# Optimization experiments

Hardware: AMD Instinct MI355X
Metric: run time of the kernel (lower is better)

The kernel has to match this reference:

```python
import jax, jax.numpy as jnp
import numpy as np

B, T, D_IN, H, NUM_OUT = 64, 2048, 128, 512, 128


def _lstm_layer(x, W_ih, W_hh, b_ih, b_hh):
    # x: [B, T, D]; W_ih: [4H, D]; W_hh: [4H, H]; gate order i, f, g, o (PyTorch)
    Bsz = x.shape[0]
    Hh = W_hh.shape[1]
    # Precompute the input projection for all timesteps in one big GEMM: [B, T, 4H]
    xg = jnp.einsum('btd,gd->btg', x, W_ih) + b_ih + b_hh
    h0 = jnp.zeros((Bsz, Hh), x.dtype)
    c0 = jnp.zeros((Bsz, Hh), x.dtype)

    def step(carry, xg_t):
        h, c = carry
        gates = xg_t + h @ W_hh.T  # [B, 4H]
        i, f, g, o = jnp.split(gates, 4, axis=-1)
        i = jax.nn.sigmoid(i)
        f = jax.nn.sigmoid(f)
        g = jnp.tanh(g)
        o = jax.nn.sigmoid(o)
        c = f * c + i * g
        h = o * jnp.tanh(c)
        return (h, c), h

    (_, _), hs = jax.lax.scan(step, (h0, c0), jnp.swapaxes(xg, 0, 1))  # hs: [T, B, H]
    return jnp.swapaxes(hs, 0, 1)  # [B, T, H]


def setup_inputs() -> dict:
    key = jax.random.key(0)
    ks = jax.random.split(key, 7)

    def xavier(k, shape):
        fan_in, fan_out = shape[1], shape[0]
        lim = np.sqrt(6.0 / (fan_in + fan_out))
        return jax.random.uniform(k, shape, jnp.float32, -lim, lim)

    return {
        'x': jax.random.normal(ks[0], (B, T, D_IN), jnp.float32),
        'W_ih0': xavier(ks[1], (4 * H, D_IN)),
        'W_hh0': xavier(ks[2], (4 * H, H)),
        'b_ih0': jnp.zeros((4 * H,), jnp.float32),
        'b_hh0': jnp.zeros((4 * H,), jnp.float32),
        'W_ih1': xavier(ks[3], (4 * H, H)),
        'W_hh1': xavier(ks[4], (4 * H, H)),
        'b_ih1': jnp.zeros((4 * H,), jnp.float32),
        'b_hh1': jnp.zeros((4 * H,), jnp.float32),
        'fc_w': xavier(ks[5], (NUM_OUT, H)),
        'fc_b': jnp.zeros((NUM_OUT,), jnp.float32),
    }


def reference(x, W_ih0, W_hh0, b_ih0, b_hh0, W_ih1, W_hh1, b_ih1, b_hh1, fc_w, fc_b):
    out = _lstm_layer(x, W_ih0, W_hh0, b_ih0, b_hh0)
    out = _lstm_layer(out, W_ih1, W_hh1, b_ih1, b_hh1)
    # fc applied to last timestep only
    return out[:, -1, :] @ fc_w.T + fc_b
```

## Files before the change

### kernel.cpp

```cpp
#include <hip/hip_runtime.h>
#include <hip/hip_fp16.h>
#include <math.h>

#define BB    64
#define TT    2048
#define DIN   128
#define HH    512
#define NWG   256
#define NTHR  256
#define NUNITS 1152

typedef __attribute__((ext_vector_type(4))) unsigned int u32x4;
typedef __attribute__((ext_vector_type(8))) _Float16    f16x8;
typedef __attribute__((ext_vector_type(4))) float       f32x4;

__device__ __forceinline__ float sigm(float v) { return 1.0f / (1.0f + expf(-v)); }

__device__ __forceinline__ u32x4 ld16m(const void* p) {
  u32x4 v;
  asm volatile("global_load_dwordx4 %0, %1, off sc0 sc1" : "=v"(v) : "v"(p) : "memory");
  return v;
}
__device__ __forceinline__ void st8m(void* p, unsigned long long v) {
  __hip_atomic_store((unsigned long long*)p, v, __ATOMIC_RELAXED, __HIP_MEMORY_SCOPE_AGENT);
}
__device__ __forceinline__ unsigned long long ld8m(const void* p) {
  return __hip_atomic_load((const unsigned long long*)p, __ATOMIC_RELAXED, __HIP_MEMORY_SCOPE_AGENT);
}
__device__ __forceinline__ void gbar(unsigned* cnt, unsigned target, int* dead) {
  __syncthreads();
  if (threadIdx.x == 0 && *dead == 0) {
    asm volatile("s_waitcnt vmcnt(0)" ::: "memory");
    __hip_atomic_fetch_add(cnt, 1u, __ATOMIC_RELAXED, __HIP_MEMORY_SCOPE_AGENT);
    long sp = 0;
    while (__hip_atomic_load(cnt, __ATOMIC_RELAXED, __HIP_MEMORY_SCOPE_AGENT) < target) {
      __builtin_amdgcn_s_sleep(1);
      if (++sp > (1L << 22)) { *dead = 1; break; }
    }
    asm volatile("" ::: "memory");
  }
  __syncthreads();
}

__global__ __launch_bounds__(64, 1) void prep_flush() {
  extern __shared__ char dummy[];
  if (threadIdx.x == 0) { __threadfence(); dummy[0] = 0; }
  __syncthreads();
}
__global__ void prep_zero(unsigned* w) {
  const int total = (4*BB*HH*2 + 4096) / 4;
  for (int i = blockIdx.x*blockDim.x + threadIdx.x; i < total; i += gridDim.x*blockDim.x)
    __hip_atomic_store(w + i, 0u, __ATOMIC_RELAXED, __HIP_MEMORY_SCOPE_AGENT);
}
__global__ void xcvt(const float* __restrict__ x, unsigned long long* __restrict__ xh) {
  const int N4 = BB*TT*DIN/4;
  const float4* x4 = reinterpret_cast<const float4*>(x);
  for (int i = blockIdx.x*blockDim.x + threadIdx.x; i < N4; i += gridDim.x*blockDim.x) {
    float4 v = x4[i];
    __half2 a = __floats2half2_rn(v.x, v.y);
    __half2 b = __floats2half2_rn(v.z, v.w);
    unsigned long long u = ((unsigned long long)__builtin_bit_cast(unsigned, b) << 32)
                         |  (unsigned long long)__builtin_bit_cast(unsigned, a);
    __hip_atomic_store(&xh[i], u, __ATOMIC_RELAXED, __HIP_MEMORY_SCOPE_AGENT);
  }
}

__global__ __launch_bounds__(NTHR, 1) void lstm2_ntr(
    const float* __restrict__ Wih0, const float* __restrict__ Whh0,
    const float* __restrict__ bih0, const float* __restrict__ bhh0,
    const float* __restrict__ Wih1, const float* __restrict__ Whh1,
    const float* __restrict__ bih1, const float* __restrict__ bhh1,
    const float* __restrict__ fcw,  const float* __restrict__ fcb,
    float* __restrict__ out, float* __restrict__ ws)
{
  extern __shared__ char smbase[];
  const int tid  = threadIdx.x;
  const int wg   = blockIdx.x;
  const int lane = tid & 63;
  const int wv   = tid >> 6;

  const int grp  = wg >> 5;
  const int r    = wg & 31;
  const int bg8  = grp * 8;
  const int c0   = 16*r + 4*wv;

  __half* h0s = reinterpret_cast<__half*>(ws);
  __half* h1s = h0s + 2*BB*HH;
  unsigned* gcnt = reinterpret_cast<unsigned*>(reinterpret_cast<char*>(ws) + 262144) + grp*32;
  const __half* xh = reinterpret_cast<const __half*>(reinterpret_cast<char*>(ws) + 524288);
  __half* hout = reinterpret_cast<__half*>(smbase + 18432);
  int*    dead = reinterpret_cast<int*>(smbase + 18944);

  const int rt   = lane & 15;
  const int gate = rt & 3;
  const int jc   = rt >> 2;
  const int kg   = lane >> 4;
  const int b15  = lane & 15;
  const int n0   = gate*HH + (c0 + jc);

  f16x8 af0[20];
#pragma unroll
  for (int m = 0; m < 20; ++m) {
    int k0 = 32*m + 8*kg;
    const float* srcp = (k0 < DIN) ? (Wih0 + (size_t)n0*DIN + k0)
                                   : (Whh0 + (size_t)n0*HH + (k0 - DIN));
    float4 a = *reinterpret_cast<const float4*>(srcp);
    float4 b = *reinterpret_cast<const float4*>(srcp + 4);
    f16x8 fr;
    fr[0]=(_Float16)a.x; fr[1]=(_Float16)a.y; fr[2]=(_Float16)a.z; fr[3]=(_Float16)a.w;
    fr[4]=(_Float16)b.x; fr[5]=(_Float16)b.y; fr[6]=(_Float16)b.z; fr[7]=(_Float16)b.w;
    af0[m] = fr;
  }
  f16x8 af1[32];
#pragma unroll
  for (int m = 0; m < 32; ++m) {
    int k0 = 32*m + 8*kg;
    const float* srcp = (k0 < HH) ? (Wih1 + (size_t)n0*HH + k0)
                                  : (Whh1 + (size_t)n0*HH + (k0 - HH));
    float4 a = *reinterpret_cast<const float4*>(srcp);
    float4 b = *reinterpret_cast<const float4*>(srcp + 4);
    f16x8 fr;
    fr[0]=(_Float16)a.x; fr[1]=(_Float16)a.y; fr[2]=(_Float16)a.z; fr[3]=(_Float16)a.w;
    fr[4]=(_Float16)b.x; fr[5]=(_Float16)b.y; fr[6]=(_Float16)b.z; fr[7]=(_Float16)b.w;
    af1[m] = fr;
  }

  const int cmy = c0 + kg;
  float bv0[4], bv1[4];
#pragma unroll
  for (int g = 0; g < 4; ++g) {
    bv0[g] = bih0[g*HH + cmy] + bhh0[g*HH + cmy];
    bv1[g] = bih1[g*HH + cmy] + bhh1[g*HH + cmy];
  }

  float cst0 = 0.f, cst1 = 0.f;
  const int beff = (b15 < 8) ? b15 : 7;
  if (tid == 0) *dead = 0;
  __syncthreads();

  for (int st = 0; st <= TT; ++st) {
    const int tcur = (st < TT) ? st : (TT - 1);
    const __half* h0r = h0s + (st & 1)*(BB*HH);
    const __half* h1r = h1s + (st & 1)*(BB*HH);

    u32x4 stgL[5];
    int   physv[5];
#pragma unroll
    for (int ii = 0; ii < 5; ++ii) {
      int idx = tid + NTHR*ii;
      physv[ii] = -1;
      if (idx < NUNITS) {
        const __half* src; int phys;
        if (idx < 128)      { int b = idx>>4, u = idx&15;
          src = xh + (size_t)(bg8+b)*TT*DIN + (size_t)tcur*DIN + u*8;
          phys = b*16 + (u ^ b); }
        else if (idx < 640) { int i2 = idx-128, b = i2>>6, u = i2&63;
          src = h0r + (size_t)(bg8+b)*HH + u*8;
          phys = 128 + b*64 + (u ^ b); }
        else                { int i2 = idx-640, b = i2>>6, u = i2&63;
          src = h1r + (size_t)(bg8+b)*HH + u*8;
          phys = 640 + b*64 + (u ^ b); }
        physv[ii] = phys;
        stgL[ii] = ld16m(src);
      }
    }
    asm volatile("s_waitcnt vmcnt(0)" ::: "memory");
    __builtin_amdgcn_sched_barrier(0);
#pragma unroll
    for (int ii = 0; ii < 5; ++ii)
      if (physv[ii] >= 0)
        *reinterpret_cast<u32x4*>(smbase + physv[ii]*16) = stgL[ii];
    __syncthreads();

    f32x4 a0a = {0.f,0.f,0.f,0.f}, a0b = a0a, a1a = a0a, a1b = a0a;
#pragma unroll
    for (int m = 0; m < 20; ++m) {
      int phys = (m < 4) ? (beff*16 + ((4*m + kg) ^ beff))
                         : (128 + beff*64 + ((4*(m-4) + kg) ^ beff));
      f16x8 bf = *reinterpret_cast<const f16x8*>(smbase + phys*16);
      if (m & 1) a0b = __builtin_amdgcn_mfma_f32_16x16x32_f16(af0[m], bf, a0b, 0, 0, 0);
      else       a0a = __builtin_amdgcn_mfma_f32_16x16x32_f16(af0[m], bf, a0a, 0, 0, 0);
    }
#pragma unroll
    for (int m = 0; m < 32; ++m) {
      int phys = (m < 16) ? (128 + beff*64 + ((4*m + kg) ^ beff))
                          : (640 + beff*64 + ((4*(m-16) + kg) ^ beff));
      f16x8 bf = *reinterpret_cast<const f16x8*>(smbase + phys*16);
      if (m & 1) a1b = __builtin_amdgcn_mfma_f32_16x16x32_f16(af1[m], bf, a1b, 0, 0, 0);
      else       a1a = __builtin_amdgcn_mfma_f32_16x16x32_f16(af1[m], bf, a1a, 0, 0, 0);
    }
    f32x4 a0 = a0a + a0b;
    f32x4 a1 = a1a + a1b;

    if (st < TT) {
      float gi = sigm (a0[0] + bv0[0]);
      float gf = sigm (a0[1] + bv0[1]);
      float gg = tanhf(a0[2] + bv0[2]);
      float go = sigm (a0[3] + bv0[3]);
      cst0 = gf*cst0 + gi*gg;
      float hn = go * tanhf(cst0);
      if (b15 < 8) hout[(0*8 + b15)*16 + 4*wv + kg] = __float2half(hn);
    }
    if (st >= 1) {
      float gi = sigm (a1[0] + bv1[0]);
      float gf = sigm (a1[1] + bv1[1]);
      float gg = tanhf(a1[2] + bv1[2]);
      float go = sigm (a1[3] + bv1[3]);
      cst1 = gf*cst1 + gi*gg;
      float hn = go * tanhf(cst1);
      if (b15 < 8) hout[(1*8 + b15)*16 + 4*wv + kg] = __float2half(hn);
    }
    __syncthreads();

    if (tid < 64) {
      int layer = tid >> 5, q = tid & 31, b = q >> 2, part = q & 3;
      bool do_st = (layer == 0) ? (st < TT) : (st >= 1);
      if (do_st) {
        unsigned long long v =
            *reinterpret_cast<unsigned long long*>(hout + (layer*8 + b)*16 + part*4);
        __half* base = (layer ? h1s : h0s) + ((st + 1) & 1)*(BB*HH);
        st8m(base + (size_t)(bg8+b)*HH + 16*r + part*4, v);
      }
    }
    gbar(gcnt, 32u*(unsigned)(st + 1), dead);
  }

  {
    const __half* h1f = h1s + (BB*HH);
    int oi = tid >> 3, kp = tid & 7;
    int b  = oi >> 2, cc = oi & 3;
    int ocol = 4*r + cc;
    const unsigned long long* h8 =
        reinterpret_cast<const unsigned long long*>(h1f + (size_t)(bg8+b)*HH) + kp*16;
    const float* wrow = fcw + (size_t)ocol*HH + kp*64;
    float p = 0.f;
#pragma unroll
    for (int kk = 0; kk < 16; ++kk) {
      unsigned long long v = ld8m(h8 + kk);
      __half2 hlo = __builtin_bit_cast(__half2, (unsigned)(v & 0xffffffffull));
      __half2 hhi = __builtin_bit_cast(__half2, (unsigned)(v >> 32));
      float2 flo = __half22float2(hlo), fhi = __half22float2(hhi);
      float4 w = *reinterpret_cast<const float4*>(wrow + kk*4);
      p += flo.x*w.x + flo.y*w.y + fhi.x*w.z + fhi.y*w.w;
    }
    p += __shfl_xor(p, 1);
    p += __shfl_xor(p, 2);
    p += __shfl_xor(p, 4);
    if (kp == 0) out[(size_t)(bg8+b)*128 + ocol] = p + fcb[ocol];
  }
}

__global__ void sentinel_fail(float* out, float v) { out[threadIdx.x] = v; }

extern "C" void kernel_launch(void* const* d_in, const int* in_sizes, int n_in,
                              void* d_out, int out_size, void* d_ws, size_t ws_size,
                              hipStream_t stream) {
  const float* x    = (const float*)d_in[0];
  const float* Wih0 = (const float*)d_in[1];
  const float* Whh0 = (const float*)d_in[2];
  const float* bih0 = (const float*)d_in[3];
  const float* bhh0 = (const float*)d_in[4];
  const float* Wih1 = (const float*)d_in[5];
  const float* Whh1 = (const float*)d_in[6];
  const float* bih1 = (const float*)d_in[7];
  const float* bhh1 = (const float*)d_in[8];
  const float* fcw  = (const float*)d_in[9];
  const float* fcb  = (const float*)d_in[10];
  float* out = (float*)d_out;
  float* ws  = (float*)d_ws;
  (void)in_sizes; (void)n_in; (void)out_size;

  const size_t need = 524288 + (size_t)BB*TT*DIN*2;
  if (ws_size < need) {
    sentinel_fail<<<1, 128, 0, stream>>>(out, 2.0e6f);
    return;
  }

  const int smem_bytes = 108*1024;
  hipFuncSetAttribute(reinterpret_cast<const void*>(&lstm2_ntr),
                      hipFuncAttributeMaxDynamicSharedMemorySize, smem_bytes);
  hipFuncSetAttribute(reinterpret_cast<const void*>(&prep_flush),
                      hipFuncAttributeMaxDynamicSharedMemorySize, smem_bytes);

  (void)hipGetLastError();
  prep_flush<<<dim3(NWG), dim3(64), smem_bytes, stream>>>();
  xcvt<<<dim3(2048), dim3(NTHR), 0, stream>>>(
      x, reinterpret_cast<unsigned long long*>(reinterpret_cast<char*>(d_ws) + 524288));
  prep_zero<<<dim3(NWG), dim3(NTHR), 0, stream>>>((unsigned*)d_ws);
  lstm2_ntr<<<dim3(NWG), dim3(NTHR), smem_bytes, stream>>>(
      Wih0, Whh0, bih0, bhh0, Wih1, Whh1, bih1, bhh1, fcw, fcb, out, ws);
  hipError_t e = hipGetLastError();
  if (e != hipSuccess) {
    sentinel_fail<<<1, 128, 0, stream>>>(out, 1.0e6f);
  }
}
```

Before: 8.324 ms.

## Split global barrier into per-layer arrive/poll and overlap layer-1 with layer-0 wait

Replaces the single per-step group barrier with two counters, one per layer. Each workgroup now computes layer-1 from a double-buffered LDS copy of the previous step while waiting for layer-0 hidden states. Layer-1 hidden states use a triple-buffered global array, so the layer-0 critical path only waits on layer-0 producers. The aim is to hide barrier latency and global load latency behind MFMA work, at the cost of an extra loop iteration, more syncthreads and more complex buffer indexing.

New measurement: 9.803 ms. +17.8%, slower.

```diff
diff --git a/kernel.cpp b/kernel.cpp
--- a/kernel.cpp
+++ b/kernel.cpp
@@ -8,38 +8,34 @@
 #define HH    512
 #define NWG   256
 #define NTHR  256
-#define NUNITS 1152
 
 typedef __attribute__((ext_vector_type(4))) unsigned int u32x4;
 typedef __attribute__((ext_vector_type(8))) _Float16    f16x8;
 typedef __attribute__((ext_vector_type(4))) float       f32x4;
+typedef unsigned long long u64;
 
 __device__ __forceinline__ float sigm(float v) { return 1.0f / (1.0f + expf(-v)); }
 
-__device__ __forceinline__ u32x4 ld16m(const void* p) {
-  u32x4 v;
-  asm volatile("global_load_dwordx4 %0, %1, off sc0 sc1" : "=v"(v) : "v"(p) : "memory");
-  return v;
-}
-__device__ __forceinline__ void st8m(void* p, unsigned long long v) {
-  __hip_atomic_store((unsigned long long*)p, v, __ATOMIC_RELAXED, __HIP_MEMORY_SCOPE_AGENT);
-}
-__device__ __forceinline__ unsigned long long ld8m(const void* p) {
-  return __hip_atomic_load((const unsigned long long*)p, __ATOMIC_RELAXED, __HIP_MEMORY_SCOPE_AGENT);
-}
-__device__ __forceinline__ void gbar(unsigned* cnt, unsigned target, int* dead) {
-  __syncthreads();
-  if (threadIdx.x == 0 && *dead == 0) {
-    asm volatile("s_waitcnt vmcnt(0)" ::: "memory");
-    __hip_atomic_fetch_add(cnt, 1u, __ATOMIC_RELAXED, __HIP_MEMORY_SCOPE_AGENT);
-    long sp = 0;
-    while (__hip_atomic_load(cnt, __ATOMIC_RELAXED, __HIP_MEMORY_SCOPE_AGENT) < target) {
-      __builtin_amdgcn_s_sleep(1);
-      if (++sp > (1L << 22)) { *dead = 1; break; }
-    }
-    asm volatile("" ::: "memory");
-  }
-  __syncthreads();
+__device__ __forceinline__ u64 ald(const void* p) {
+  return __hip_atomic_load((const u64*)p, __ATOMIC_RELAXED, __HIP_MEMORY_SCOPE_AGENT);
+}
+__device__ __forceinline__ void ast(void* p, u64 v) {
+  __hip_atomic_store((u64*)p, v, __ATOMIC_RELAXED, __HIP_MEMORY_SCOPE_AGENT);
+}
+__device__ __forceinline__ void put16(char* dst, u64 lo, u64 hi) {
+  u32x4 v; v.x=(unsigned)lo; v.y=(unsigned)(lo>>32); v.z=(unsigned)hi; v.w=(unsigned)(hi>>32);
+  *reinterpret_cast<u32x4*>(dst) = v;
+}
+__device__ __forceinline__ void barrive(unsigned* cnt) {
+  __hip_atomic_fetch_add(cnt, 1u, __ATOMIC_RELAXED, __HIP_MEMORY_SCOPE_AGENT);
+}
+__device__ __forceinline__ void bpoll(unsigned* cnt, unsigned target, int* dead) {
+  if (*dead) return;
+  long sp = 0;
+  while (__hip_atomic_load(cnt, __ATOMIC_RELAXED, __HIP_MEMORY_SCOPE_AGENT) < target) {
+    __builtin_amdgcn_s_sleep(1);
+    if (++sp > (1L << 22)) { *dead = 1; break; }
+  }
 }
 
 __global__ __launch_bounds__(64, 1) void prep_flush() {
@@ -48,24 +44,23 @@
   __syncthreads();
 }
 __global__ void prep_zero(unsigned* w) {
-  const int total = (4*BB*HH*2 + 4096) / 4;
+  const int total = (131072 + 196608 + 4096) / 4;
   for (int i = blockIdx.x*blockDim.x + threadIdx.x; i < total; i += gridDim.x*blockDim.x)
     __hip_atomic_store(w + i, 0u, __ATOMIC_RELAXED, __HIP_MEMORY_SCOPE_AGENT);
 }
-__global__ void xcvt(const float* __restrict__ x, unsigned long long* __restrict__ xh) {
+__global__ void xcvt(const float* __restrict__ x, u64* __restrict__ xh) {
   const int N4 = BB*TT*DIN/4;
   const float4* x4 = reinterpret_cast<const float4*>(x);
   for (int i = blockIdx.x*blockDim.x + threadIdx.x; i < N4; i += gridDim.x*blockDim.x) {
     float4 v = x4[i];
     __half2 a = __floats2half2_rn(v.x, v.y);
     __half2 b = __floats2half2_rn(v.z, v.w);
-    unsigned long long u = ((unsigned long long)__builtin_bit_cast(unsigned, b) << 32)
-                         |  (unsigned long long)__builtin_bit_cast(unsigned, a);
+    u64 u = ((u64)__builtin_bit_cast(unsigned, b) << 32) | (u64)__builtin_bit_cast(unsigned, a);
     __hip_atomic_store(&xh[i], u, __ATOMIC_RELAXED, __HIP_MEMORY_SCOPE_AGENT);
   }
 }
 
-__global__ __launch_bounds__(NTHR, 1) void lstm2_ntr(
+__global__ __launch_bounds__(NTHR, 1) void lstm2_lp2(
     const float* __restrict__ Wih0, const float* __restrict__ Whh0,
     const float* __restrict__ bih0, const float* __restrict__ bhh0,
     const float* __restrict__ Wih1, const float* __restrict__ Whh1,
@@ -74,22 +69,26 @@
     float* __restrict__ out, float* __restrict__ ws)
 {
   extern __shared__ char smbase[];
+  char* buf0 = smbase;
+  char* buf1 = smbase + 18432;
+  __half* hout = reinterpret_cast<__half*>(smbase + 36864);
+  int*    dead = reinterpret_cast<int*>(smbase + 37376);
+
   const int tid  = threadIdx.x;
   const int wg   = blockIdx.x;
   const int lane = tid & 63;
   const int wv   = tid >> 6;
-
   const int grp  = wg >> 5;
   const int r    = wg & 31;
   const int bg8  = grp * 8;
   const int c0   = 16*r + 4*wv;
 
   __half* h0s = reinterpret_cast<__half*>(ws);
-  __half* h1s = h0s + 2*BB*HH;
-  unsigned* gcnt = reinterpret_cast<unsigned*>(reinterpret_cast<char*>(ws) + 262144) + grp*32;
-  const __half* xh = reinterpret_cast<const __half*>(reinterpret_cast<char*>(ws) + 524288);
-  __half* hout = reinterpret_cast<__half*>(smbase + 18432);
-  int*    dead = reinterpret_cast<int*>(smbase + 18944);
+  __half* h1s = reinterpret_cast<__half*>((char*)ws + 131072);
+  unsigned* barb = reinterpret_cast<unsigned*>((char*)ws + 327680);
+  unsigned* gA = barb + grp*32;
+  unsigned* gB = barb + 512 + grp*32;
+  const __half* xh = reinterpret_cast<const __half*>((char*)ws + 524288);
 
   const int rt   = lane & 15;
   const int gate = rt & 3;
@@ -136,107 +135,132 @@
   float cst0 = 0.f, cst1 = 0.f;
   const int beff = (b15 < 8) ? b15 : 7;
   if (tid == 0) *dead = 0;
+
+  if (tid < 128) {
+    int b = tid >> 4, u = tid & 15;
+    const __half* s_ = xh + (size_t)(bg8+b)*TT*DIN + (size_t)0*DIN + u*8;
+    u64 lo = ald(s_), hi = ald(s_ + 4);
+    put16(buf0 + (b*16 + (u^b))*16, lo, hi);
+  }
   __syncthreads();
 
-  for (int st = 0; st <= TT; ++st) {
-    const int tcur = (st < TT) ? st : (TT - 1);
-    const __half* h0r = h0s + (st & 1)*(BB*HH);
-    const __half* h1r = h1s + (st & 1)*(BB*HH);
-
-    u32x4 stgL[5];
-    int   physv[5];
-#pragma unroll
-    for (int ii = 0; ii < 5; ++ii) {
-      int idx = tid + NTHR*ii;
-      physv[ii] = -1;
-      if (idx < NUNITS) {
-        const __half* src; int phys;
-        if (idx < 128)      { int b = idx>>4, u = idx&15;
-          src = xh + (size_t)(bg8+b)*TT*DIN + (size_t)tcur*DIN + u*8;
-          phys = b*16 + (u ^ b); }
-        else if (idx < 640) { int i2 = idx-128, b = i2>>6, u = i2&63;
-          src = h0r + (size_t)(bg8+b)*HH + u*8;
-          phys = 128 + b*64 + (u ^ b); }
-        else                { int i2 = idx-640, b = i2>>6, u = i2&63;
-          src = h1r + (size_t)(bg8+b)*HH + u*8;
-          phys = 640 + b*64 + (u ^ b); }
-        physv[ii] = phys;
-        stgL[ii] = ld16m(src);
+  for (int st = 0; st <= TT + 1; ++st) {
+    char* bufc = (st & 1) ? buf1 : buf0;
+    char* bufp = (st & 1) ? buf0 : buf1;
+
+    if (tid == 0) bpoll(gA, 32u*(unsigned)st, dead);
+    __syncthreads();
+
+    const __half* h0r = h0s + (size_t)(st & 1)*BB*HH;
+    u64 a0, a1, a2, a3;
+    { int idx = tid;       int b = idx>>6, u = idx&63;
+      const __half* s_ = h0r + (size_t)(bg8+b)*HH + u*8; a0 = ald(s_); a1 = ald(s_+4); }
+    { int idx = tid + 256; int b = idx>>6, u = idx&63;
+      const __half* s_ = h0r + (size_t)(bg8+b)*HH + u*8; a2 = ald(s_); a3 = ald(s_+4); }
+    __builtin_amdgcn_sched_barrier(0);
+
+    if (st >= 2) {
+      f32x4 p1a = {0.f,0.f,0.f,0.f}, p1b = p1a;
+#pragma unroll
+      for (int m = 0; m < 32; ++m) {
+        int phys = (m < 16) ? (128 + beff*64 + ((4*m + kg) ^ beff))
+                            : (640 + beff*64 + ((4*(m-16) + kg) ^ beff));
+        f16x8 bf = *reinterpret_cast<const f16x8*>(bufp + phys*16);
+        if (m & 1) p1b = __builtin_amdgcn_mfma_f32_16x16x32_f16(af1[m], bf, p1b, 0, 0, 0);
+        else       p1a = __builtin_amdgcn_mfma_f32_16x16x32_f16(af1[m], bf, p1a, 0, 0, 0);
       }
-    }
+      f32x4 av = p1a + p1b;
+      float gi = sigm (av[0] + bv1[0]);
+      float gf = sigm (av[1] + bv1[1]);
+      float gg = tanhf(av[2] + bv1[2]);
+      float go = sigm (av[3] + bv1[3]);
+      cst1 = gf*cst1 + gi*gg;
+      float hn = go * tanhf(cst1);
+      if (b15 < 8) hout[(8 + b15)*16 + 4*wv + kg] = __float2half(hn);
+    }
+    __syncthreads();
+    if (st >= 2 && tid < 32) {
+      int b = tid >> 2, part = tid & 3;
+      u64 v = *reinterpret_cast<u64*>(hout + (8 + b)*16 + part*4);
+      __half* base = h1s + (size_t)((st + 1) % 3)*BB*HH;
+      ast(base + (size_t)(bg8+b)*HH + 16*r + part*4, v);
+    }
+
+    { int idx = tid;       int b = idx>>6, u = idx&63;
+      put16(bufc + (128 + b*64 + (u^b))*16, a0, a1); }
+    { int idx = tid + 256; int b = idx>>6, u = idx&63;
+      put16(bufc + (128 + b*64 + (u^b))*16, a2, a3); }
     asm volatile("s_waitcnt vmcnt(0)" ::: "memory");
-    __builtin_amdgcn_sched_barrier(0);
-#pragma unroll
-    for (int ii = 0; ii < 5; ++ii)
-      if (physv[ii] >= 0)
-        *reinterpret_cast<u32x4*>(smbase + physv[ii]*16) = stgL[ii];
-    __syncthreads();
-
-    f32x4 a0a = {0.f,0.f,0.f,0.f}, a0b = a0a, a1a = a0a, a1b = a0a;
-#pragma unroll
-    for (int m = 0; m < 20; ++m) {
-      int phys = (m < 4) ? (beff*16 + ((4*m + kg) ^ beff))
-                         : (128 + beff*64 + ((4*(m-4) + kg) ^ beff));
-      f16x8 bf = *reinterpret_cast<const f16x8*>(smbase + phys*16);
-      if (m & 1) a0b = __builtin_amdgcn_mfma_f32_16x16x32_f16(af0[m], bf, a0b, 0, 0, 0);
-      else       a0a = __builtin_amdgcn_mfma_f32_16x16x32_f16(af0[m], bf, a0a, 0, 0, 0);
-    }
-#pragma unroll
-    for (int m = 0; m < 32; ++m) {
-      int phys = (m < 16) ? (128 + beff*64 + ((4*m + kg) ^ beff))
-                          : (640 + beff*64 + ((4*(m-16) + kg) ^ beff));
-      f16x8 bf = *reinterpret_cast<const f16x8*>(smbase + phys*16);
-      if (m & 1) a1b = __builtin_amdgcn_mfma_f32_16x16x32_f16(af1[m], bf, a1b, 0, 0, 0);
-      else       a1a = __builtin_amdgcn_mfma_f32_16x16x32_f16(af1[m], bf, a1a, 0, 0, 0);
-    }
-    f32x4 a0 = a0a + a0b;
-    f32x4 a1 = a1a + a1b;
+    if (tid == 0 && st >= 2) barrive(gB);
+    __syncthreads();
 
     if (st < TT) {
-      float gi = sigm (a0[0] + bv0[0]);
-      float gf = sigm (a0[1] + bv0[1]);
-      float gg = tanhf(a0[2] + bv0[2]);
-      float go = sigm (a0[3] + bv0[3]);
+      f32x4 p0a = {0.f,0.f,0.f,0.f}, p0b = p0a;
+#pragma unroll
+      for (int m = 0; m < 20; ++m) {
+        int phys = (m < 4) ? (beff*16 + ((4*m + kg) ^ beff))
+                           : (128 + beff*64 + ((4*(m-4) + kg) ^ beff));
+        f16x8 bf = *reinterpret_cast<const f16x8*>(bufc + phys*16);
+        if (m & 1) p0b = __builtin_amdgcn_mfma_f32_16x16x32_f16(af0[m], bf, p0b, 0, 0, 0);
+        else       p0a = __builtin_amdgcn_mfma_f32_16x16x32_f16(af0[m], bf, p0a, 0, 0, 0);
+      }
+      f32x4 av = p0a + p0b;
+      float gi = sigm (av[0] + bv0[0]);
+      float gf = sigm (av[1] + bv0[1]);
+      float gg = tanhf(av[2] + bv0[2]);
+      float go = sigm (av[3] + bv0[3]);
       cst0 = gf*cst0 + gi*gg;
       float hn = go * tanhf(cst0);
-      if (b15 < 8) hout[(0*8 + b15)*16 + 4*wv + kg] = __float2half(hn);
-    }
-    if (st >= 1) {
-      float gi = sigm (a1[0] + bv1[0]);
-      float gf = sigm (a1[1] + bv1[1]);
-      float gg = tanhf(a1[2] + bv1[2]);
-      float go = sigm (a1[3] + bv1[3]);
-      cst1 = gf*cst1 + gi*gg;
-      float hn = go * tanhf(cst1);
-      if (b15 < 8) hout[(1*8 + b15)*16 + 4*wv + kg] = __float2half(hn);
-    }
-    __syncthreads();
-
-    if (tid < 64) {
-      int layer = tid >> 5, q = tid & 31, b = q >> 2, part = q & 3;
-      bool do_st = (layer == 0) ? (st < TT) : (st >= 1);
-      if (do_st) {
-        unsigned long long v =
-            *reinterpret_cast<unsigned long long*>(hout + (layer*8 + b)*16 + part*4);
-        __half* base = (layer ? h1s : h0s) + ((st + 1) & 1)*(BB*HH);
-        st8m(base + (size_t)(bg8+b)*HH + 16*r + part*4, v);
-      }
-    }
-    gbar(gcnt, 32u*(unsigned)(st + 1), dead);
+      if (b15 < 8) hout[b15*16 + 4*wv + kg] = __float2half(hn);
+    }
+    __syncthreads();
+    if (st < TT && tid < 32) {
+      int b = tid >> 2, part = tid & 3;
+      u64 v = *reinterpret_cast<u64*>(hout + b*16 + part*4);
+      __half* base = h0s + (size_t)((st+1) & 1)*BB*HH;
+      ast(base + (size_t)(bg8+b)*HH + 16*r + part*4, v);
+    }
+    asm volatile("s_waitcnt vmcnt(0)" ::: "memory");
+    if (tid == 0) barrive(gA);
+
+    {
+      unsigned tgtB = (st >= 1) ? 32u*(unsigned)(st - 1) : 0u;
+      if (tid == 0) bpoll(gB, tgtB, dead);
+    }
+    __syncthreads();
+    {
+      const __half* hb = h1s + (size_t)((st + 1) % 3)*BB*HH;
+      int tx = (st+1 < TT) ? (st+1) : (TT-1);
+      u64 e0, e1, e2, e3, e4 = 0, e5 = 0;
+      { int idx = tid;       int b = idx>>6, u = idx&63;
+        const __half* s_ = hb + (size_t)(bg8+b)*HH + u*8; e0 = ald(s_); e1 = ald(s_+4); }
+      { int idx = tid + 256; int b = idx>>6, u = idx&63;
+        const __half* s_ = hb + (size_t)(bg8+b)*HH + u*8; e2 = ald(s_); e3 = ald(s_+4); }
+      const bool hx = (tid < 128);
+      if (hx) { int b = tid>>4, u = tid&15;
+        const __half* s_ = xh + (size_t)(bg8+b)*TT*DIN + (size_t)tx*DIN + u*8;
+        e4 = ald(s_); e5 = ald(s_+4); }
+      { int idx = tid;       int b = idx>>6, u = idx&63;
+        put16(bufc + (640 + b*64 + (u^b))*16, e0, e1); }
+      { int idx = tid + 256; int b = idx>>6, u = idx&63;
+        put16(bufc + (640 + b*64 + (u^b))*16, e2, e3); }
+      if (hx) { int b = tid>>4, u = tid&15;
+        put16(bufp + (b*16 + (u^b))*16, e4, e5); }
+    }
+    __syncthreads();
   }
 
   {
-    const __half* h1f = h1s + (BB*HH);
+    const __half* h1f = h1s + (size_t)((TT-1) % 3)*BB*HH;
     int oi = tid >> 3, kp = tid & 7;
     int b  = oi >> 2, cc = oi & 3;
     int ocol = 4*r + cc;
-    const unsigned long long* h8 =
-        reinterpret_cast<const unsigned long long*>(h1f + (size_t)(bg8+b)*HH) + kp*16;
+    const u64* h8 = reinterpret_cast<const u64*>(h1f + (size_t)(bg8+b)*HH) + kp*16;
     const float* wrow = fcw + (size_t)ocol*HH + kp*64;
     float p = 0.f;
 #pragma unroll
     for (int kk = 0; kk < 16; ++kk) {
-      unsigned long long v = ld8m(h8 + kk);
+      u64 v = ald(h8 + kk);
       __half2 hlo = __builtin_bit_cast(__half2, (unsigned)(v & 0xffffffffull));
       __half2 hhi = __builtin_bit_cast(__half2, (unsigned)(v >> 32));
       float2 flo = __half22float2(hlo), fhi = __half22float2(hhi);
@@ -277,7 +301,7 @@
   }
 
   const int smem_bytes = 108*1024;
-  hipFuncSetAttribute(reinterpret_cast<const void*>(&lstm2_ntr),
+  hipFuncSetAttribute(reinterpret_cast<const void*>(&lstm2_lp2),
                       hipFuncAttributeMaxDynamicSharedMemorySize, smem_bytes);
   hipFuncSetAttribute(reinterpret_cast<const void*>(&prep_flush),
                       hipFuncAttributeMaxDynamicSharedMemorySize, smem_bytes);
@@ -285,9 +309,9 @@
   (void)hipGetLastError();
   prep_flush<<<dim3(NWG), dim3(64), smem_bytes, stream>>>();
   xcvt<<<dim3(2048), dim3(NTHR), 0, stream>>>(
-      x, reinterpret_cast<unsigned long long*>(reinterpret_cast<char*>(d_ws) + 524288));
+      x, reinterpret_cast<u64*>(reinterpret_cast<char*>(d_ws) + 524288));
   prep_zero<<<dim3(NWG), dim3(NTHR), 0, stream>>>((unsigned*)d_ws);
-  lstm2_ntr<<<dim3(NWG), dim3(NTHR), smem_bytes, stream>>>(
+  lstm2_lp2<<<dim3(NWG), dim3(NTHR), smem_bytes, stream>>>(
       Wih0, Whh0, bih0, bhh0, Wih1, Whh1, bih1, bhh1, fcw, fcb, out, ws);
   hipError_t e = hipGetLastError();
   if (e != hipSuccess) {
```

## Split batch across twice as many workgroups with two WGs per CU

Applied to the files above, without the earlier changes.

Doubles the grid to 512 workgroups, each handling 4 batch rows instead of 8, halves shared memory to allow two workgroups per CU, and adjusts staging, swizzle offsets, h-output writes and the final FC reduction to match. The aim is to shrink per-step staging work and latency on the recurrent critical path and to overlap two workgroups per CU. The cost is that the MFMA B-operand is now only a quarter used (4 of 16 columns), weights are duplicated across twice as many workgroups, and co-residency of all 512 persistent workgroups is required for the grid barrier to avoid deadlock.

After: 27.07 ms. 3.25x slower.

```diff
diff --git a/kernel.cpp b/kernel.cpp
--- a/kernel.cpp
+++ b/kernel.cpp
@@ -6,13 +6,14 @@
 #define TT    2048
 #define DIN   128
 #define HH    512
-#define NWG   256
+#define NWG   512
 #define NTHR  256
-#define NUNITS 1152
+#define NUNITS 576
 
 typedef __attribute__((ext_vector_type(4))) unsigned int u32x4;
 typedef __attribute__((ext_vector_type(8))) _Float16    f16x8;
 typedef __attribute__((ext_vector_type(4))) float       f32x4;
+typedef unsigned long long u64;
 
 __device__ __forceinline__ float sigm(float v) { return 1.0f / (1.0f + expf(-v)); }
 
@@ -21,11 +22,11 @@
   asm volatile("global_load_dwordx4 %0, %1, off sc0 sc1" : "=v"(v) : "v"(p) : "memory");
   return v;
 }
-__device__ __forceinline__ void st8m(void* p, unsigned long long v) {
-  __hip_atomic_store((unsigned long long*)p, v, __ATOMIC_RELAXED, __HIP_MEMORY_SCOPE_AGENT);
-}
-__device__ __forceinline__ unsigned long long ld8m(const void* p) {
-  return __hip_atomic_load((const unsigned long long*)p, __ATOMIC_RELAXED, __HIP_MEMORY_SCOPE_AGENT);
+__device__ __forceinline__ void st8m(void* p, u64 v) {
+  __hip_atomic_store((u64*)p, v, __ATOMIC_RELAXED, __HIP_MEMORY_SCOPE_AGENT);
+}
+__device__ __forceinline__ u64 ld8m(const void* p) {
+  return __hip_atomic_load((const u64*)p, __ATOMIC_RELAXED, __HIP_MEMORY_SCOPE_AGENT);
 }
 __device__ __forceinline__ void gbar(unsigned* cnt, unsigned target, int* dead) {
   __syncthreads();
@@ -52,20 +53,19 @@
   for (int i = blockIdx.x*blockDim.x + threadIdx.x; i < total; i += gridDim.x*blockDim.x)
     __hip_atomic_store(w + i, 0u, __ATOMIC_RELAXED, __HIP_MEMORY_SCOPE_AGENT);
 }
-__global__ void xcvt(const float* __restrict__ x, unsigned long long* __restrict__ xh) {
+__global__ void xcvt(const float* __restrict__ x, u64* __restrict__ xh) {
   const int N4 = BB*TT*DIN/4;
   const float4* x4 = reinterpret_cast<const float4*>(x);
   for (int i = blockIdx.x*blockDim.x + threadIdx.x; i < N4; i += gridDim.x*blockDim.x) {
     float4 v = x4[i];
     __half2 a = __floats2half2_rn(v.x, v.y);
     __half2 b = __floats2half2_rn(v.z, v.w);
-    unsigned long long u = ((unsigned long long)__builtin_bit_cast(unsigned, b) << 32)
-                         |  (unsigned long long)__builtin_bit_cast(unsigned, a);
+    u64 u = ((u64)__builtin_bit_cast(unsigned, b) << 32) | (u64)__builtin_bit_cast(unsigned, a);
     __hip_atomic_store(&xh[i], u, __ATOMIC_RELAXED, __HIP_MEMORY_SCOPE_AGENT);
   }
 }
 
-__global__ __launch_bounds__(NTHR, 1) void lstm2_ntr(
+__global__ __launch_bounds__(NTHR, 2) void lstm2_tlp(
     const float* __restrict__ Wih0, const float* __restrict__ Whh0,
     const float* __restrict__ bih0, const float* __restrict__ bhh0,
     const float* __restrict__ Wih1, const float* __restrict__ Whh1,
@@ -74,6 +74,9 @@
     float* __restrict__ out, float* __restrict__ ws)
 {
   extern __shared__ char smbase[];
+  __half* hout = reinterpret_cast<__half*>(smbase + 9216);
+  int*    dead = reinterpret_cast<int*>(smbase + 9216 + 256);
+
   const int tid  = threadIdx.x;
   const int wg   = blockIdx.x;
   const int lane = tid & 63;
@@ -81,15 +84,13 @@
 
   const int grp  = wg >> 5;
   const int r    = wg & 31;
-  const int bg8  = grp * 8;
+  const int bg4  = grp * 4;
   const int c0   = 16*r + 4*wv;
 
   __half* h0s = reinterpret_cast<__half*>(ws);
   __half* h1s = h0s + 2*BB*HH;
   unsigned* gcnt = reinterpret_cast<unsigned*>(reinterpret_cast<char*>(ws) + 262144) + grp*32;
   const __half* xh = reinterpret_cast<const __half*>(reinterpret_cast<char*>(ws) + 524288);
-  __half* hout = reinterpret_cast<__half*>(smbase + 18432);
-  int*    dead = reinterpret_cast<int*>(smbase + 18944);
 
   const int rt   = lane & 15;
   const int gate = rt & 3;
@@ -134,32 +135,32 @@
   }
 
   float cst0 = 0.f, cst1 = 0.f;
-  const int beff = (b15 < 8) ? b15 : 7;
+  const int beff = (b15 < 4) ? b15 : 3;
   if (tid == 0) *dead = 0;
   __syncthreads();
 
   for (int st = 0; st <= TT; ++st) {
     const int tcur = (st < TT) ? st : (TT - 1);
-    const __half* h0r = h0s + (st & 1)*(BB*HH);
-    const __half* h1r = h1s + (st & 1)*(BB*HH);
-
-    u32x4 stgL[5];
-    int   physv[5];
-#pragma unroll
-    for (int ii = 0; ii < 5; ++ii) {
+    const __half* h0r = h0s + (size_t)(st & 1)*BB*HH;
+    const __half* h1r = h1s + (size_t)(st & 1)*BB*HH;
+
+    u32x4 stgL[3];
+    int   physv[3];
+#pragma unroll
+    for (int ii = 0; ii < 3; ++ii) {
       int idx = tid + NTHR*ii;
       physv[ii] = -1;
       if (idx < NUNITS) {
         const __half* src; int phys;
-        if (idx < 128)      { int b = idx>>4, u = idx&15;
-          src = xh + (size_t)(bg8+b)*TT*DIN + (size_t)tcur*DIN + u*8;
+        if (idx < 64)       { int b = idx>>4, u = idx&15;
+          src = xh + (size_t)(bg4+b)*TT*DIN + (size_t)tcur*DIN + u*8;
           phys = b*16 + (u ^ b); }
-        else if (idx < 640) { int i2 = idx-128, b = i2>>6, u = i2&63;
-          src = h0r + (size_t)(bg8+b)*HH + u*8;
-          phys = 128 + b*64 + (u ^ b); }
-        else                { int i2 = idx-640, b = i2>>6, u = i2&63;
-          src = h1r + (size_t)(bg8+b)*HH + u*8;
-          phys = 640 + b*64 + (u ^ b); }
+        else if (idx < 320) { int i2 = idx-64,  b = i2>>6, u = i2&63;
+          src = h0r + (size_t)(bg4+b)*HH + u*8;
+          phys = 64 + b*64 + (u ^ b); }
+        else                { int i2 = idx-320, b = i2>>6, u = i2&63;
+          src = h1r + (size_t)(bg4+b)*HH + u*8;
+          phys = 320 + b*64 + (u ^ b); }
         physv[ii] = phys;
         stgL[ii] = ld16m(src);
       }
@@ -167,7 +168,7 @@
     asm volatile("s_waitcnt vmcnt(0)" ::: "memory");
     __builtin_amdgcn_sched_barrier(0);
 #pragma unroll
-    for (int ii = 0; ii < 5; ++ii)
+    for (int ii = 0; ii < 3; ++ii)
       if (physv[ii] >= 0)
         *reinterpret_cast<u32x4*>(smbase + physv[ii]*16) = stgL[ii];
     __syncthreads();
@@ -176,15 +177,15 @@
 #pragma unroll
     for (int m = 0; m < 20; ++m) {
       int phys = (m < 4) ? (beff*16 + ((4*m + kg) ^ beff))
-                         : (128 + beff*64 + ((4*(m-4) + kg) ^ beff));
+                         : (64 + beff*64 + ((4*(m-4) + kg) ^ beff));
       f16x8 bf = *reinterpret_cast<const f16x8*>(smbase + phys*16);
       if (m & 1) a0b = __builtin_amdgcn_mfma_f32_16x16x32_f16(af0[m], bf, a0b, 0, 0, 0);
       else       a0a = __builtin_amdgcn_mfma_f32_16x16x32_f16(af0[m], bf, a0a, 0, 0, 0);
     }
 #pragma unroll
     for (int m = 0; m < 32; ++m) {
-      int phys = (m < 16) ? (128 + beff*64 + ((4*m + kg) ^ beff))
-                          : (640 + beff*64 + ((4*(m-16) + kg) ^ beff));
+      int phys = (m < 16) ? (64 + beff*64 + ((4*m + kg) ^ beff))
+                          : (320 + beff*64 + ((4*(m-16) + kg) ^ beff));
       f16x8 bf = *reinterpret_cast<const f16x8*>(smbase + phys*16);
       if (m & 1) a1b = __builtin_amdgcn_mfma_f32_16x16x32_f16(af1[m], bf, a1b, 0, 0, 0);
       else       a1a = __builtin_amdgcn_mfma_f32_16x16x32_f16(af1[m], bf, a1a, 0, 0, 0);
@@ -199,7 +200,7 @@
       float go = sigm (a0[3] + bv0[3]);
       cst0 = gf*cst0 + gi*gg;
       float hn = go * tanhf(cst0);
-      if (b15 < 8) hout[(0*8 + b15)*16 + 4*wv + kg] = __float2half(hn);
+      if (b15 < 4) hout[0*64 + b15*16 + 4*wv + kg] = __float2half(hn);
     }
     if (st >= 1) {
       float gi = sigm (a1[0] + bv1[0]);
@@ -208,35 +209,33 @@
       float go = sigm (a1[3] + bv1[3]);
       cst1 = gf*cst1 + gi*gg;
       float hn = go * tanhf(cst1);
-      if (b15 < 8) hout[(1*8 + b15)*16 + 4*wv + kg] = __float2half(hn);
+      if (b15 < 4) hout[1*64 + b15*16 + 4*wv + kg] = __float2half(hn);
     }
     __syncthreads();
 
-    if (tid < 64) {
-      int layer = tid >> 5, q = tid & 31, b = q >> 2, part = q & 3;
+    if (tid < 32) {
+      int layer = tid >> 4, q = tid & 15, b = q >> 2, part = q & 3;
       bool do_st = (layer == 0) ? (st < TT) : (st >= 1);
       if (do_st) {
-        unsigned long long v =
-            *reinterpret_cast<unsigned long long*>(hout + (layer*8 + b)*16 + part*4);
-        __half* base = (layer ? h1s : h0s) + ((st + 1) & 1)*(BB*HH);
-        st8m(base + (size_t)(bg8+b)*HH + 16*r + part*4, v);
+        u64 v = *reinterpret_cast<u64*>(hout + layer*64 + b*16 + part*4);
+        __half* base = (layer ? h1s : h0s) + (size_t)((st + 1) & 1)*BB*HH;
+        st8m(base + (size_t)(bg4+b)*HH + 16*r + part*4, v);
       }
     }
     gbar(gcnt, 32u*(unsigned)(st + 1), dead);
   }
 
   {
-    const __half* h1f = h1s + (BB*HH);
-    int oi = tid >> 3, kp = tid & 7;
+    const __half* h1f = h1s + (size_t)BB*HH;
+    int oi = tid >> 4, kp = tid & 15;
     int b  = oi >> 2, cc = oi & 3;
     int ocol = 4*r + cc;
-    const unsigned long long* h8 =
-        reinterpret_cast<const unsigned long long*>(h1f + (size_t)(bg8+b)*HH) + kp*16;
-    const float* wrow = fcw + (size_t)ocol*HH + kp*64;
+    const u64* h8 = reinterpret_cast<const u64*>(h1f + (size_t)(bg4+b)*HH) + kp*8;
+    const float* wrow = fcw + (size_t)ocol*HH + kp*32;
     float p = 0.f;
 #pragma unroll
-    for (int kk = 0; kk < 16; ++kk) {
-      unsigned long long v = ld8m(h8 + kk);
+    for (int kk = 0; kk < 8; ++kk) {
+      u64 v = ld8m(h8 + kk);
       __half2 hlo = __builtin_bit_cast(__half2, (unsigned)(v & 0xffffffffull));
       __half2 hhi = __builtin_bit_cast(__half2, (unsigned)(v >> 32));
       float2 flo = __half22float2(hlo), fhi = __half22float2(hhi);
@@ -246,7 +245,8 @@
     p += __shfl_xor(p, 1);
     p += __shfl_xor(p, 2);
     p += __shfl_xor(p, 4);
-    if (kp == 0) out[(size_t)(bg8+b)*128 + ocol] = p + fcb[ocol];
+    p += __shfl_xor(p, 8);
+    if (kp == 0) out[(size_t)(bg4+b)*128 + ocol] = p + fcb[ocol];
   }
 }
 
@@ -276,18 +276,19 @@
     return;
   }
 
-  const int smem_bytes = 108*1024;
-  hipFuncSetAttribute(reinterpret_cast<const void*>(&lstm2_ntr),
-                      hipFuncAttributeMaxDynamicSharedMemorySize, smem_bytes);
+  const int flush_smem = 108*1024;
+  const int main_smem  = 54*1024;
+  hipFuncSetAttribute(reinterpret_cast<const void*>(&lstm2_tlp),
+                      hipFuncAttributeMaxDynamicSharedMemorySize, main_smem);
   hipFuncSetAttribute(reinterpret_cast<const void*>(&prep_flush),
-                      hipFuncAttributeMaxDynamicSharedMemorySize, smem_bytes);
+                      hipFuncAttributeMaxDynamicSharedMemorySize, flush_smem);
 
   (void)hipGetLastError();
-  prep_flush<<<dim3(NWG), dim3(64), smem_bytes, stream>>>();
+  prep_flush<<<dim3(256), dim3(64), flush_smem, stream>>>();
   xcvt<<<dim3(2048), dim3(NTHR), 0, stream>>>(
-      x, reinterpret_cast<unsigned long long*>(reinterpret_cast<char*>(d_ws) + 524288));
-  prep_zero<<<dim3(NWG), dim3(NTHR), 0, stream>>>((unsigned*)d_ws);
-  lstm2_ntr<<<dim3(NWG), dim3(NTHR), smem_bytes, stream>>>(
+      x, reinterpret_cast<u64*>(reinterpret_cast<char*>(d_ws) + 524288));
+  prep_zero<<<dim3(256), dim3(NTHR), 0, stream>>>((unsigned*)d_ws);
+  lstm2_tlp<<<dim3(NWG), dim3(NTHR), main_smem, stream>>>(
       Wih0, Whh0, bih0, bhh0, Wih1, Whh1, bih1, bhh1, fcw, fcb, out, ws);
   hipError_t e = hipGetLastError();
   if (e != hipSuccess) {
```

## Replace atomic counter barrier with per-workgroup flag array polled by a wave

Applied to the files above, without the earlier changes.

The group barrier changes from a shared fetch-add counter spun on by one thread to a per-workgroup flag store. A whole wavefront polls all 32 flags of its group at once and checks them with a wave-wide all-reduce. This removes contention from 32 atomic increments on one address per step, at the cost of 32 loads per poll iteration. The LDS XOR swizzle also changes to use the batch index shifted left by one, aiming to cut bank conflicts on the fragment reads.

Result: no change. 8.455 ms (+1.6%).

```diff
diff --git a/kernel.cpp b/kernel.cpp
--- a/kernel.cpp
+++ b/kernel.cpp
@@ -13,6 +13,7 @@
 typedef __attribute__((ext_vector_type(4))) unsigned int u32x4;
 typedef __attribute__((ext_vector_type(8))) _Float16    f16x8;
 typedef __attribute__((ext_vector_type(4))) float       f32x4;
+typedef unsigned long long u64;
 
 __device__ __forceinline__ float sigm(float v) { return 1.0f / (1.0f + expf(-v)); }
 
@@ -21,25 +22,11 @@
   asm volatile("global_load_dwordx4 %0, %1, off sc0 sc1" : "=v"(v) : "v"(p) : "memory");
   return v;
 }
-__device__ __forceinline__ void st8m(void* p, unsigned long long v) {
-  __hip_atomic_store((unsigned long long*)p, v, __ATOMIC_RELAXED, __HIP_MEMORY_SCOPE_AGENT);
-}
-__device__ __forceinline__ unsigned long long ld8m(const void* p) {
-  return __hip_atomic_load((const unsigned long long*)p, __ATOMIC_RELAXED, __HIP_MEMORY_SCOPE_AGENT);
-}
-__device__ __forceinline__ void gbar(unsigned* cnt, unsigned target, int* dead) {
-  __syncthreads();
-  if (threadIdx.x == 0 && *dead == 0) {
-    asm volatile("s_waitcnt vmcnt(0)" ::: "memory");
-    __hip_atomic_fetch_add(cnt, 1u, __ATOMIC_RELAXED, __HIP_MEMORY_SCOPE_AGENT);
-    long sp = 0;
-    while (__hip_atomic_load(cnt, __ATOMIC_RELAXED, __HIP_MEMORY_SCOPE_AGENT) < target) {
-      __builtin_amdgcn_s_sleep(1);
-      if (++sp > (1L << 22)) { *dead = 1; break; }
-    }
-    asm volatile("" ::: "memory");
-  }
-  __syncthreads();
+__device__ __forceinline__ void st8m(void* p, u64 v) {
+  __hip_atomic_store((u64*)p, v, __ATOMIC_RELAXED, __HIP_MEMORY_SCOPE_AGENT);
+}
+__device__ __forceinline__ u64 ld8m(const void* p) {
+  return __hip_atomic_load((const u64*)p, __ATOMIC_RELAXED, __HIP_MEMORY_SCOPE_AGENT);
 }
 
 __global__ __launch_bounds__(64, 1) void prep_flush() {
@@ -48,24 +35,23 @@
   __syncthreads();
 }
 __global__ void prep_zero(unsigned* w) {
-  const int total = (4*BB*HH*2 + 4096) / 4;
+  const int total = (4*BB*HH*2 + 8192) / 4;
   for (int i = blockIdx.x*blockDim.x + threadIdx.x; i < total; i += gridDim.x*blockDim.x)
     __hip_atomic_store(w + i, 0u, __ATOMIC_RELAXED, __HIP_MEMORY_SCOPE_AGENT);
 }
-__global__ void xcvt(const float* __restrict__ x, unsigned long long* __restrict__ xh) {
+__global__ void xcvt(const float* __restrict__ x, u64* __restrict__ xh) {
   const int N4 = BB*TT*DIN/4;
   const float4* x4 = reinterpret_cast<const float4*>(x);
   for (int i = blockIdx.x*blockDim.x + threadIdx.x; i < N4; i += gridDim.x*blockDim.x) {
     float4 v = x4[i];
     __half2 a = __floats2half2_rn(v.x, v.y);
     __half2 b = __floats2half2_rn(v.z, v.w);
-    unsigned long long u = ((unsigned long long)__builtin_bit_cast(unsigned, b) << 32)
-                         |  (unsigned long long)__builtin_bit_cast(unsigned, a);
+    u64 u = ((u64)__builtin_bit_cast(unsigned, b) << 32) | (u64)__builtin_bit_cast(unsigned, a);
     __hip_atomic_store(&xh[i], u, __ATOMIC_RELAXED, __HIP_MEMORY_SCOPE_AGENT);
   }
 }
 
-__global__ __launch_bounds__(NTHR, 1) void lstm2_ntr(
+__global__ __launch_bounds__(NTHR, 1) void lstm2_fb(
     const float* __restrict__ Wih0, const float* __restrict__ Whh0,
     const float* __restrict__ bih0, const float* __restrict__ bhh0,
     const float* __restrict__ Wih1, const float* __restrict__ Whh1,
@@ -74,6 +60,9 @@
     float* __restrict__ out, float* __restrict__ ws)
 {
   extern __shared__ char smbase[];
+  __half* hout = reinterpret_cast<__half*>(smbase + 18432);
+  int*    dead = reinterpret_cast<int*>(smbase + 18944);
+
   const int tid  = threadIdx.x;
   const int wg   = blockIdx.x;
   const int lane = tid & 63;
@@ -86,10 +75,8 @@
 
   __half* h0s = reinterpret_cast<__half*>(ws);
   __half* h1s = h0s + 2*BB*HH;
-  unsigned* gcnt = reinterpret_cast<unsigned*>(reinterpret_cast<char*>(ws) + 262144) + grp*32;
-  const __half* xh = reinterpret_cast<const __half*>(reinterpret_cast<char*>(ws) + 524288);
-  __half* hout = reinterpret_cast<__half*>(smbase + 18432);
-  int*    dead = reinterpret_cast<int*>(smbase + 18944);
+  unsigned* flg = reinterpret_cast<unsigned*>((char*)ws + 262144) + grp*32;
+  const __half* xh = reinterpret_cast<const __half*>((char*)ws + 524288);
 
   const int rt   = lane & 15;
   const int gate = rt & 3;
@@ -135,13 +122,14 @@
 
   float cst0 = 0.f, cst1 = 0.f;
   const int beff = (b15 < 8) ? b15 : 7;
+  const int bsw  = beff << 1;
   if (tid == 0) *dead = 0;
   __syncthreads();
 
   for (int st = 0; st <= TT; ++st) {
     const int tcur = (st < TT) ? st : (TT - 1);
-    const __half* h0r = h0s + (st & 1)*(BB*HH);
-    const __half* h1r = h1s + (st & 1)*(BB*HH);
+    const __half* h0r = h0s + (size_t)(st & 1)*BB*HH;
+    const __half* h1r = h1s + (size_t)(st & 1)*BB*HH;
 
     u32x4 stgL[5];
     int   physv[5];
@@ -153,13 +141,13 @@
         const __half* src; int phys;
         if (idx < 128)      { int b = idx>>4, u = idx&15;
           src = xh + (size_t)(bg8+b)*TT*DIN + (size_t)tcur*DIN + u*8;
-          phys = b*16 + (u ^ b); }
+          phys = b*16 + (u ^ ((b<<1)&15)); }
         else if (idx < 640) { int i2 = idx-128, b = i2>>6, u = i2&63;
           src = h0r + (size_t)(bg8+b)*HH + u*8;
-          phys = 128 + b*64 + (u ^ b); }
+          phys = 128 + b*64 + (u ^ (b<<1)); }
         else                { int i2 = idx-640, b = i2>>6, u = i2&63;
           src = h1r + (size_t)(bg8+b)*HH + u*8;
-          phys = 640 + b*64 + (u ^ b); }
+          phys = 640 + b*64 + (u ^ (b<<1)); }
         physv[ii] = phys;
         stgL[ii] = ld16m(src);
       }
@@ -175,16 +163,16 @@
     f32x4 a0a = {0.f,0.f,0.f,0.f}, a0b = a0a, a1a = a0a, a1b = a0a;
 #pragma unroll
     for (int m = 0; m < 20; ++m) {
-      int phys = (m < 4) ? (beff*16 + ((4*m + kg) ^ beff))
-                         : (128 + beff*64 + ((4*(m-4) + kg) ^ beff));
+      int phys = (m < 4) ? (beff*16 + ((4*m + kg) ^ (bsw & 15)))
+                         : (128 + beff*64 + ((4*(m-4) + kg) ^ bsw));
       f16x8 bf = *reinterpret_cast<const f16x8*>(smbase + phys*16);
       if (m & 1) a0b = __builtin_amdgcn_mfma_f32_16x16x32_f16(af0[m], bf, a0b, 0, 0, 0);
       else       a0a = __builtin_amdgcn_mfma_f32_16x16x32_f16(af0[m], bf, a0a, 0, 0, 0);
     }
 #pragma unroll
     for (int m = 0; m < 32; ++m) {
-      int phys = (m < 16) ? (128 + beff*64 + ((4*m + kg) ^ beff))
-                          : (640 + beff*64 + ((4*(m-16) + kg) ^ beff));
+      int phys = (m < 16) ? (128 + beff*64 + ((4*m + kg) ^ bsw))
+                          : (640 + beff*64 + ((4*(m-16) + kg) ^ bsw));
       f16x8 bf = *reinterpret_cast<const f16x8*>(smbase + phys*16);
       if (m & 1) a1b = __builtin_amdgcn_mfma_f32_16x16x32_f16(af1[m], bf, a1b, 0, 0, 0);
       else       a1a = __builtin_amdgcn_mfma_f32_16x16x32_f16(af1[m], bf, a1a, 0, 0, 0);
@@ -216,27 +204,44 @@
       int layer = tid >> 5, q = tid & 31, b = q >> 2, part = q & 3;
       bool do_st = (layer == 0) ? (st < TT) : (st >= 1);
       if (do_st) {
-        unsigned long long v =
-            *reinterpret_cast<unsigned long long*>(hout + (layer*8 + b)*16 + part*4);
-        __half* base = (layer ? h1s : h0s) + ((st + 1) & 1)*(BB*HH);
+        u64 v = *reinterpret_cast<u64*>(hout + (layer*8 + b)*16 + part*4);
+        __half* base = (layer ? h1s : h0s) + (size_t)((st + 1) & 1)*BB*HH;
         st8m(base + (size_t)(bg8+b)*HH + 16*r + part*4, v);
       }
     }
-    gbar(gcnt, 32u*(unsigned)(st + 1), dead);
+
+    __syncthreads();
+    if (wv == 0 && *dead == 0) {
+      asm volatile("s_waitcnt vmcnt(0)" ::: "memory");
+      if (lane == 0)
+        __hip_atomic_store(flg + r, (unsigned)(st + 1),
+                           __ATOMIC_RELAXED, __HIP_MEMORY_SCOPE_AGENT);
+      long sp = 0;
+      for (;;) {
+        unsigned f = 0u;
+        if (lane < 32)
+          f = __hip_atomic_load(flg + lane, __ATOMIC_RELAXED, __HIP_MEMORY_SCOPE_AGENT);
+        bool ok = (lane < 32) ? (f >= (unsigned)(st + 1)) : true;
+        if (__all(ok)) break;
+        __builtin_amdgcn_s_sleep(1);
+        if (++sp > (1L << 22)) { if (lane == 0) *dead = 1; break; }
+      }
+      asm volatile("" ::: "memory");
+    }
+    __syncthreads();
   }
 
   {
-    const __half* h1f = h1s + (BB*HH);
+    const __half* h1f = h1s + (size_t)BB*HH;
     int oi = tid >> 3, kp = tid & 7;
     int b  = oi >> 2, cc = oi & 3;
     int ocol = 4*r + cc;
-    const unsigned long long* h8 =
-        reinterpret_cast<const unsigned long long*>(h1f + (size_t)(bg8+b)*HH) + kp*16;
+    const u64* h8 = reinterpret_cast<const u64*>(h1f + (size_t)(bg8+b)*HH) + kp*16;
     const float* wrow = fcw + (size_t)ocol*HH + kp*64;
     float p = 0.f;
 #pragma unroll
     for (int kk = 0; kk < 16; ++kk) {
-      unsigned long long v = ld8m(h8 + kk);
+      u64 v = ld8m(h8 + kk);
       __half2 hlo = __builtin_bit_cast(__half2, (unsigned)(v & 0xffffffffull));
       __half2 hhi = __builtin_bit_cast(__half2, (unsigned)(v >> 32));
       float2 flo = __half22float2(hlo), fhi = __half22float2(hhi);
@@ -277,7 +282,7 @@
   }
 
   const int smem_bytes = 108*1024;
-  hipFuncSetAttribute(reinterpret_cast<const void*>(&lstm2_ntr),
+  hipFuncSetAttribute(reinterpret_cast<const void*>(&lstm2_fb),
                       hipFuncAttributeMaxDynamicSharedMemorySize, smem_bytes);
   hipFuncSetAttribute(reinterpret_cast<const void*>(&prep_flush),
                       hipFuncAttributeMaxDynamicSharedMemorySize, smem_bytes);
@@ -285,9 +290,9 @@
   (void)hipGetLastError();
   prep_flush<<<dim3(NWG), dim3(64), smem_bytes, stream>>>();
   xcvt<<<dim3(2048), dim3(NTHR), 0, stream>>>(
-      x, reinterpret_cast<unsigned long long*>(reinterpret_cast<char*>(d_ws) + 524288));
+      x, reinterpret_cast<u64*>(reinterpret_cast<char*>(d_ws) + 524288));
   prep_zero<<<dim3(NWG), dim3(NTHR), 0, stream>>>((unsigned*)d_ws);
-  lstm2_ntr<<<dim3(NWG), dim3(NTHR), smem_bytes, stream>>>(
+  lstm2_fb<<<dim3(NWG), dim3(NTHR), smem_bytes, stream>>>(
       Wih0, Whh0, bih0, bhh0, Wih1, Whh1, bih1, bhh1, fcw, fcb, out, ws);
   hipError_t e = hipGetLastError();
   if (e != hipSuccess) {
```
